# Optimization experiments

Hardware: AMD Instinct MI355X
Metric: run time of the kernel (lower is better)

The kernel has to match this reference:

```python
import jax, jax.numpy as jnp
import numpy as np

B, S, D = 4, 4096, 2048
G, EPG = 4, 16          # num_groups, experts_per_group
E = G * EPG             # num_experts = 64
H = 64                  # complexity estimator hidden


def setup_inputs() -> dict:
    key = jax.random.key(0)
    ks = jax.random.split(key, 7)
    scale = 0.02
    return {
        "x": jax.random.normal(ks[0], (B, S, D), dtype=jnp.float32),
        "Wg": jax.random.normal(ks[1], (G, D), dtype=jnp.float32) * scale,
        "We": jax.random.normal(ks[2], (G, EPG, D), dtype=jnp.float32) * scale,
        "W1": jax.random.normal(ks[3], (H, D), dtype=jnp.float32) * scale,
        "b1": jax.random.normal(ks[4], (H,), dtype=jnp.float32) * scale,
        "W2": jax.random.normal(ks[5], (1, H), dtype=jnp.float32) * scale,
        "b2": jax.random.normal(ks[6], (1,), dtype=jnp.float32) * scale,
        "min_experts": 1,
        "max_experts": 2,
    }


def _router_forward(x, Wg, We, W1, b1, W2, b2, min_experts, max_experts):
    # complexity estimator: Linear -> ReLU -> Linear -> Sigmoid, squeeze(-1)
    h = jax.nn.relu(jnp.einsum("bsd,hd->bsh", x, W1) + b1)
    complexity = jax.nn.sigmoid(jnp.einsum("bsh,oh->bso", h, W2) + b2)[..., 0]  # [B,S]
    # torch: clamp((score * max_experts).int(), min, max); .int() truncates (floor for >=0)
    k = jnp.clip((complexity * max_experts).astype(jnp.int32), min_experts, max_experts)  # [B,S]

    # group routing
    group_logits = jnp.einsum("bsd,gd->bsg", x, Wg)          # [B,S,G]
    group_probs = jax.nn.softmax(group_logits, axis=-1)
    gidx = jnp.argmax(group_probs, axis=-1)                   # [B,S]

    # per-group expert logits for all groups, then pick the chosen group per token
    expert_logits_all = jnp.einsum("bsd,ged->bsge", x, We)    # [B,S,G,EPG]
    expert_logits = jnp.take_along_axis(
        expert_logits_all, gidx[:, :, None, None], axis=2
    )[:, :, 0, :]                                             # [B,S,EPG]
    expert_probs = jax.nn.softmax(expert_logits, axis=-1)     # [B,S,EPG]

    # per-token top-k (k in {1,2}); always take top-2, mask the 2nd when k==1
    topv, topi = jax.lax.top_k(expert_probs, max_experts)     # [B,S,2]
    use2 = (k >= 2).astype(topv.dtype)                        # [B,S]
    mask = jnp.stack([jnp.ones_like(use2), use2], axis=-1)    # [B,S,2]
    denom = jnp.sum(topv * mask, axis=-1, keepdims=True)
    norm_probs = topv * mask / denom                          # [B,S,2]

    flat_idx = gidx[:, :, None] * EPG + topi                  # [B,S,2] global expert ids
    oh = jax.nn.one_hot(flat_idx, E, dtype=x.dtype)           # [B,S,2,E]
    dispatch = jnp.sum(oh * mask[..., None], axis=2)          # [B,S,E]
    combine = jnp.sum(oh * norm_probs[..., None], axis=2)     # [B,S,E]

    # router_probs: group_prob[gidx] * expert_probs scattered into chosen group's slice
    gp_max = jnp.take_along_axis(group_probs, gidx[..., None], axis=-1)[..., 0]  # [B,S]
    oh_g = jax.nn.one_hot(gidx, G, dtype=x.dtype)             # [B,S,G]
    router_probs = (oh_g[..., :, None] * (gp_max[..., None] * expert_probs)[..., None, :]
                    ).reshape(x.shape[0], x.shape[1], E)      # [B,S,E]

    denom_tok = x.shape[0] * x.shape[1]
    router_prob_per_expert = jnp.sum(router_probs, axis=(0, 1)) / denom_tok
    expert_usage = jnp.sum(dispatch, axis=(0, 1)) / denom_tok
    aux_loss = jnp.sum(router_prob_per_expert * expert_usage) * E
    return dispatch, combine, router_probs, aux_loss


def reference(x, Wg, We, W1, b1, W2, b2, min_experts, max_experts):
    return _router_forward(x, Wg, We, W1, b1, W2, b2, min_experts, max_experts)
```

## Files before the change

### kernel.cpp

```cpp
#include <hip/hip_runtime.h>
#include <cmath>

#define T_TOKENS 16384
#define DIM 2048
#define NG 4
#define EPG 16
#define NE 64
#define NJ2 68
#define NT2 5
#define NJP2 80
#define BM 256
#define KS 4
#define KSL (DIM / KS)
#define NITER (KSL / 32)
#define TAU 0.02f

#define XBUF_B 32768
#define WBUF_B 5120

typedef __attribute__((ext_vector_type(8))) short bf16x8;
typedef __attribute__((ext_vector_type(4))) float f32x4;

#define WF_FLOATS (64 * NT2 * 64 * 4)
#define P_OFF WF_FLOATS
#define P_FLOATS ((size_t)KS * T_TOKENS * NJP2)
#define SUM_OFF (P_OFF + P_FLOATS)
#define CNT_OFF (SUM_OFF + 128)
#define LIST_OFF (CNT_OFF + 4)

static __device__ inline unsigned bf16rne(float x) {
    unsigned u = __float_as_uint(x);
    return (u + 0x7FFFu + ((u >> 16) & 1u)) >> 16;
}

#define GLOAD_LDS(gsrc, ldst) \
    __builtin_amdgcn_global_load_lds( \
        (const __attribute__((address_space(1))) void*)(gsrc), \
        (__attribute__((address_space(3))) void*)(ldst), 16, 0, 0)

__global__ void moe_prep(const float* __restrict__ Wg, const float* __restrict__ We,
                         float* __restrict__ ws, float* __restrict__ sums,
                         int* __restrict__ cnt) {
    int bid = blockIdx.x;
    int kstep = bid / NT2, nt = bid % NT2;
    int lane = threadIdx.x;
    if (bid == 0) {
        sums[lane] = 0.f; sums[64 + lane] = 0.f;
        if (lane == 0) *cnt = 0;
    }
    int row = nt * 16 + (lane & 15);
    int k0 = kstep * 32 + (lane >> 4) * 8;
    const float* src = nullptr;
    if (row < NG)        src = Wg + (size_t)row * DIM;
    else if (row < NJ2)  src = We + (size_t)(row - NG) * DIM;
    unsigned r0 = 0, r1 = 0, r2 = 0, r3 = 0;
    if (src) {
        r0 = bf16rne(src[k0 + 0]) | (bf16rne(src[k0 + 1]) << 16);
        r1 = bf16rne(src[k0 + 2]) | (bf16rne(src[k0 + 3]) << 16);
        r2 = bf16rne(src[k0 + 4]) | (bf16rne(src[k0 + 5]) << 16);
        r3 = bf16rne(src[k0 + 6]) | (bf16rne(src[k0 + 7]) << 16);
    }
    ((uint4*)ws)[(size_t)(kstep * NT2 + nt) * 64 + lane] = make_uint4(r0, r1, r2, r3);
}

__global__ __launch_bounds__(512, 1) void moe_gemm(
    const float* __restrict__ x, const float* __restrict__ wfrag,
    float* __restrict__ part) {
    __shared__ __align__(16) char xs[2][XBUF_B];
    __shared__ __align__(16) char wsb[2][WBUF_B];

    const int bid = blockIdx.x;
    const int tg = bid & 63, ks = bid >> 6;
    const int tid = threadIdx.x;
    const int wave = tid >> 6, lane = tid & 63;
    const int l15 = lane & 15, lq = lane >> 4;
    const int T0 = tg * BM;
    const int K0 = ks * KSL;

    const int xtokb = wave * 32 + (lane >> 3);
    const int xp = lane & 7;
    const uint4* wg = (const uint4*)wfrag;

    const int mt0 = wave * 2;
    const int t0 = mt0 * 16 + l15;
    const int t1 = t0 + 16;

    f32x4 acc[2][NT2];
    #pragma unroll
    for (int m = 0; m < 2; ++m)
        #pragma unroll
        for (int n = 0; n < NT2; ++n) acc[m][n] = (f32x4){0.f, 0.f, 0.f, 0.f};

    auto stage = [&](int it) {
        char* xb = xs[it & 1];
        char* wb = wsb[it & 1];
        const int kf = K0 + it * 32;
        #pragma unroll
        for (int j = 0; j < 4; ++j) {
            const int tok = xtokb + j * 8;
            const float* src = x + (size_t)(T0 + tok) * DIM + kf + ((xp ^ (tok & 7)) << 2);
            GLOAD_LDS(src, xb + (wave * 256 + j * 64) * 16);
        }
        if (wave < NT2) {
            const int kstep = ks * NITER + it;
            GLOAD_LDS(wg + ((size_t)kstep * NT2 + wave) * 64 + lane, wb + wave * 1024);
        }
    };

    stage(0);
    #pragma unroll 1
    for (int it = 0; it < NITER; ++it) {
        __syncthreads();
        if (it + 1 < NITER) stage(it + 1);
        const char* xb = xs[it & 1];
        const char* wb = wsb[it & 1];

        union { unsigned u[4]; bf16x8 v; } a0, a1;
        {
            uint4 lo = *(const uint4*)(xb + t0 * 128 + (((lq * 2) ^ (t0 & 7)) << 4));
            uint4 hi = *(const uint4*)(xb + t0 * 128 + (((lq * 2 + 1) ^ (t0 & 7)) << 4));
            a0.u[0] = (lo.x >> 16) | (lo.y & 0xFFFF0000u);
            a0.u[1] = (lo.z >> 16) | (lo.w & 0xFFFF0000u);
            a0.u[2] = (hi.x >> 16) | (hi.y & 0xFFFF0000u);
            a0.u[3] = (hi.z >> 16) | (hi.w & 0xFFFF0000u);
        }
        {
            uint4 lo = *(const uint4*)(xb + t1 * 128 + (((lq * 2) ^ (t1 & 7)) << 4));
            uint4 hi = *(const uint4*)(xb + t1 * 128 + (((lq * 2 + 1) ^ (t1 & 7)) << 4));
            a1.u[0] = (lo.x >> 16) | (lo.y & 0xFFFF0000u);
            a1.u[1] = (lo.z >> 16) | (lo.w & 0xFFFF0000u);
            a1.u[2] = (hi.x >> 16) | (hi.y & 0xFFFF0000u);
            a1.u[3] = (hi.z >> 16) | (hi.w & 0xFFFF0000u);
        }
        #pragma unroll
        for (int n = 0; n < NT2; ++n) {
            bf16x8 bv = *(const bf16x8*)(wb + n * 1024 + lane * 16);
            acc[0][n] = __builtin_amdgcn_mfma_f32_16x16x32_bf16(a0.v, bv, acc[0][n], 0, 0, 0);
            acc[1][n] = __builtin_amdgcn_mfma_f32_16x16x32_bf16(a1.v, bv, acc[1][n], 0, 0, 0);
        }
    }

    float* po = part + (size_t)ks * T_TOKENS * NJP2;
    #pragma unroll
    for (int m = 0; m < 2; ++m) {
        const int tokb = T0 + (mt0 + m) * 16 + lq * 4;
        #pragma unroll
        for (int n = 0; n < NT2; ++n)
            #pragma unroll
            for (int r = 0; r < 4; ++r)
                po[(size_t)(tokb + r) * NJP2 + n * 16 + l15] = acc[m][n][r];
    }
}

__global__ __launch_bounds__(256, 2) void moe_epi(
    const float* __restrict__ part, float* __restrict__ out,
    float* __restrict__ sums, int* __restrict__ cnt, int4* __restrict__ list) {
    __shared__ float slog[16][81];
    __shared__ float rp_s[16 * 17];
    __shared__ int   sc_e1[16];
    __shared__ float s_usage[NE], s_rp[NE];

    const int tid = threadIdx.x;
    const int T0 = blockIdx.x * 16;
    if (tid < NE) { s_usage[tid] = 0.f; s_rp[tid] = 0.f; }

    for (int idx = tid; idx < 16 * NJP2; idx += 256) {
        int t = idx / NJP2, j = idx % NJP2;
        float v = part[(size_t)(T0 + t) * NJP2 + j];
        #pragma unroll
        for (int p = 1; p < KS; ++p)
            v += part[(size_t)p * T_TOKENS * NJP2 + (size_t)(T0 + t) * NJP2 + j];
        slog[t][j] = v;
    }
    __syncthreads();

    {
        const int t = tid >> 4;
        const int q = tid & 15;
        const int tok = T0 + t;
        const float* o = slog[t];

        float gl0 = o[0], gl1 = o[1], gl2 = o[2], gl3 = o[3];
        float gm = gl0; int gi = 0;
        if (gl1 > gm) { gm = gl1; gi = 1; }
        if (gl2 > gm) { gm = gl2; gi = 2; }
        if (gl3 > gm) { gm = gl3; gi = 3; }
        float g2 = -INFINITY;
        if (gi != 0 && gl0 > g2) g2 = gl0;
        if (gi != 1 && gl1 > g2) g2 = gl1;
        if (gi != 2 && gl2 > g2) g2 = gl2;
        if (gi != 3 && gl3 > g2) g2 = gl3;
        bool flagG = (gm - g2) < TAU;
        float gsum = expf(gl0 - gm) + expf(gl1 - gm) + expf(gl2 - gm) + expf(gl3 - gm);
        float gp = 1.f / gsum;

        float el = o[NG + gi * EPG + q];
        float v1v = el; int i1 = q;
        #pragma unroll
        for (int off = 8; off; off >>= 1) {
            float ov = __shfl_xor(v1v, off, 16);
            int   oi = __shfl_xor(i1, off, 16);
            if (ov > v1v || (ov == v1v && oi < i1)) { v1v = ov; i1 = oi; }
        }
        float v2v = (q == i1) ? -INFINITY : el;
        #pragma unroll
        for (int off = 8; off; off >>= 1)
            v2v = fmaxf(v2v, __shfl_xor(v2v, off, 16));
        bool flagE = (v1v - v2v) < TAU;

        float ep = expf(el - v1v);
        float es = ep;
        #pragma unroll
        for (int off = 8; off; off >>= 1) es += __shfl_xor(es, off, 16);
        float inv = 1.f / es;
        rp_s[t * 17 + q] = gp * ep * inv;

        if (q == 0) {
            sc_e1[t] = gi * EPG + i1;
            if (flagG || flagE) {
                int p = atomicAdd(cnt, 1);
                list[p] = make_int4(tok, 0, 0, 0);
            }
        }
    }
    __syncthreads();

    float* outD = out;
    float* outC = out + (size_t)T_TOKENS * NE;
    float* outR = out + (size_t)2 * T_TOKENS * NE;
    for (int idx = tid; idx < 16 * NE; idx += 256) {
        int t = idx >> 6, e = idx & 63;
        int e1i = sc_e1[t];
        int gi = e1i >> 4;
        float disp = (e == e1i) ? 1.f : 0.f;
        float rpv  = ((e >> 4) == gi) ? rp_s[t * 17 + (e & 15)] : 0.f;
        size_t ob = (size_t)(T0 + t) * NE + e;
        outD[ob] = disp; outC[ob] = disp; outR[ob] = rpv;
        atomicAdd(&s_usage[e], disp);
        atomicAdd(&s_rp[e], rpv);
    }
    __syncthreads();
    if (tid < NE) {
        atomicAdd(&sums[tid], s_usage[tid]);
        atomicAdd(&sums[NE + tid], s_rp[tid]);
    }
}

__global__ __launch_bounds__(256, 4) void moe_fix(
    const float* __restrict__ x, const float* __restrict__ Wg,
    const float* __restrict__ We, float* __restrict__ out,
    float* __restrict__ sums, const int* __restrict__ cnt,
    const int4* __restrict__ list) {
    __shared__ float gl_s[NG];
    __shared__ float el_s[EPG];
    __shared__ float rp_row[EPG];
    __shared__ int   s_gi, s_e1;
    __shared__ float s_gp;

    const int tid = threadIdx.x;
    const int wave = tid >> 6, lane = tid & 63;
    const int n = *cnt;

    for (int i = blockIdx.x; i < n; i += gridDim.x) {
        const int tok = list[i].x;
        const float* xrow = x + (size_t)tok * DIM;
        float xr[32];
        #pragma unroll
        for (int m = 0; m < 32; ++m) xr[m] = xrow[lane + m * 64];

        auto dotf = [&](const float* w) -> float {
            float s = 0.f;
            #pragma unroll
            for (int m = 0; m < 32; ++m) s = fmaf(xr[m], w[lane + m * 64], s);
            #pragma unroll
            for (int off = 32; off; off >>= 1) s += __shfl_xor(s, off, 64);
            return s;
        };

        {
            float g = dotf(Wg + (size_t)wave * DIM);
            if (lane == 0) gl_s[wave] = g;
        }
        __syncthreads();

        if (tid == 0) {
            float gm = -INFINITY; int gi = 0;
            #pragma unroll
            for (int g = 0; g < NG; ++g)
                if (gl_s[g] > gm) { gm = gl_s[g]; gi = g; }
            float gsum = 0.f;
            #pragma unroll
            for (int g = 0; g < NG; ++g) gsum += expf(gl_s[g] - gm);
            s_gp = 1.f / gsum;
            s_gi = gi;
        }
        __syncthreads();

        const int gi = s_gi;
        for (int j = wave; j < EPG; j += 4) {
            float e = dotf(We + (size_t)(gi * EPG + j) * DIM);
            if (lane == 0) el_s[j] = e;
        }
        __syncthreads();

        if (tid == 0) {
            float e1 = -INFINITY; int i1 = 0;
            #pragma unroll
            for (int j = 0; j < EPG; ++j)
                if (el_s[j] > e1) { e1 = el_s[j]; i1 = j; }
            float es = 0.f;
            #pragma unroll
            for (int j = 0; j < EPG; ++j) {
                float e = expf(el_s[j] - e1);
                rp_row[j] = e;
                es += e;
            }
            float sc = s_gp / es;
            #pragma unroll
            for (int j = 0; j < EPG; ++j) rp_row[j] *= sc;
            s_e1 = gi * EPG + i1;
        }
        __syncthreads();

        if (tid < NE) {
            const int e = tid;
            float newD = (e == s_e1) ? 1.f : 0.f;
            float newR = ((e >> 4) == gi) ? rp_row[e & 15] : 0.f;
            size_t ob = (size_t)tok * NE + e;
            float oldD = out[ob];
            float oldR = out[(size_t)2 * T_TOKENS * NE + ob];
            out[ob] = newD;
            out[(size_t)T_TOKENS * NE + ob] = newD;
            out[(size_t)2 * T_TOKENS * NE + ob] = newR;
            float dD = newD - oldD, dR = newR - oldR;
            if (dD != 0.f) atomicAdd(&sums[e], dD);
            if (dR != 0.f) atomicAdd(&sums[NE + e], dR);
        }
        __syncthreads();
    }
}

__global__ void moe_finalize(const float* __restrict__ sums, float* __restrict__ out) {
    int l = threadIdx.x;
    float v = sums[l] * sums[NE + l];
    #pragma unroll
    for (int off = 32; off; off >>= 1) v += __shfl_down(v, off, 64);
    if (l == 0) {
        float N = (float)T_TOKENS;
        out[(size_t)3 * T_TOKENS * NE] = v * (float)NE / (N * N);
    }
}

extern "C" void kernel_launch(void* const* d_in, const int* in_sizes, int n_in,
                              void* d_out, int out_size, void* d_ws, size_t ws_size,
                              hipStream_t stream) {
    const float* x  = (const float*)d_in[0];
    const float* Wg = (const float*)d_in[1];
    const float* We = (const float*)d_in[2];
    float* out = (float*)d_out;
    float* ws  = (float*)d_ws;

    float* wfrag = ws;
    float* part  = ws + P_OFF;
    float* sums  = ws + SUM_OFF;
    int*   cnt   = (int*)(ws + CNT_OFF);
    int4*  list  = (int4*)(ws + LIST_OFF);

    moe_prep<<<64 * NT2, 64, 0, stream>>>(Wg, We, wfrag, sums, cnt);
    moe_gemm<<<64 * KS, 512, 0, stream>>>(x, wfrag, part);
    moe_epi<<<T_TOKENS / 16, 256, 0, stream>>>(part, out, sums, cnt, list);
    moe_fix<<<1024, 256, 0, stream>>>(x, Wg, We, out, sums, cnt, list);
    moe_finalize<<<1, 64, 0, stream>>>(sums, out);
}
```

Before: 87.93 us.

## Shrink GEMM token tile to 64 and split N tiles across waves

Reduces the token tile per block from 256 to 64, which launches four times as many blocks with smaller LDS buffers and a launch bound that allows 4 blocks per CU. Waves are now split over 4 M-tiles and 2 halves of the N dimension (3+2 tiles), instead of each wave computing 2 M-tiles across all 5 N tiles. Block indexing is reordered so K-split blocks for the same tokens are adjacent. The aim is higher occupancy and better latency hiding for the memory-bound x stream. In exchange, each block reuses the weight fragments across fewer tokens, and the N split leaves waves with uneven MFMA work.

Result: faster. 85.38 us (-2.9%).

```diff
diff --git a/kernel.cpp b/kernel.cpp
--- a/kernel.cpp
+++ b/kernel.cpp
@@ -9,13 +9,13 @@
 #define NJ2 68
 #define NT2 5
 #define NJP2 80
-#define BM 256
+#define BM 64
 #define KS 4
 #define KSL (DIM / KS)
 #define NITER (KSL / 32)
 #define TAU 0.02f
 
-#define XBUF_B 32768
+#define XBUF_B 8192
 #define WBUF_B 5120
 
 typedef __attribute__((ext_vector_type(8))) short bf16x8;
@@ -63,44 +63,38 @@
     ((uint4*)ws)[(size_t)(kstep * NT2 + nt) * 64 + lane] = make_uint4(r0, r1, r2, r3);
 }
 
-__global__ __launch_bounds__(512, 1) void moe_gemm(
+__global__ __launch_bounds__(512, 4) void moe_gemm(
     const float* __restrict__ x, const float* __restrict__ wfrag,
     float* __restrict__ part) {
     __shared__ __align__(16) char xs[2][XBUF_B];
     __shared__ __align__(16) char wsb[2][WBUF_B];
 
     const int bid = blockIdx.x;
-    const int tg = bid & 63, ks = bid >> 6;
+    const int tg = bid >> 2, ks = bid & 3;
     const int tid = threadIdx.x;
     const int wave = tid >> 6, lane = tid & 63;
     const int l15 = lane & 15, lq = lane >> 4;
     const int T0 = tg * BM;
     const int K0 = ks * KSL;
 
-    const int xtokb = wave * 32 + (lane >> 3);
-    const int xp = lane & 7;
+    const int xtok = wave * 8 + (lane >> 3);
+    const float* xsrc = x + (size_t)(T0 + xtok) * DIM + K0
+                      + (((lane & 7) ^ (lane >> 3)) << 2);
     const uint4* wg = (const uint4*)wfrag;
 
-    const int mt0 = wave * 2;
-    const int t0 = mt0 * 16 + l15;
-    const int t1 = t0 + 16;
-
-    f32x4 acc[2][NT2];
-    #pragma unroll
-    for (int m = 0; m < 2; ++m)
-        #pragma unroll
-        for (int n = 0; n < NT2; ++n) acc[m][n] = (f32x4){0.f, 0.f, 0.f, 0.f};
+    const int mt = wave & 3, nh = wave >> 2;
+    const int ctok = mt * 16 + l15;
+    const int csw = ctok & 7;
+
+    f32x4 acc[3];
+    acc[0] = (f32x4){0.f,0.f,0.f,0.f};
+    acc[1] = (f32x4){0.f,0.f,0.f,0.f};
+    acc[2] = (f32x4){0.f,0.f,0.f,0.f};
 
     auto stage = [&](int it) {
         char* xb = xs[it & 1];
         char* wb = wsb[it & 1];
-        const int kf = K0 + it * 32;
-        #pragma unroll
-        for (int j = 0; j < 4; ++j) {
-            const int tok = xtokb + j * 8;
-            const float* src = x + (size_t)(T0 + tok) * DIM + kf + ((xp ^ (tok & 7)) << 2);
-            GLOAD_LDS(src, xb + (wave * 256 + j * 64) * 16);
-        }
+        GLOAD_LDS(xsrc + it * 32, xb + wave * 1024);
         if (wave < NT2) {
             const int kstep = ks * NITER + it;
             GLOAD_LDS(wg + ((size_t)kstep * NT2 + wave) * 64 + lane, wb + wave * 1024);
@@ -115,40 +109,41 @@
         const char* xb = xs[it & 1];
         const char* wb = wsb[it & 1];
 
-        union { unsigned u[4]; bf16x8 v; } a0, a1;
+        union { unsigned u[4]; bf16x8 v; } af;
         {
-            uint4 lo = *(const uint4*)(xb + t0 * 128 + (((lq * 2) ^ (t0 & 7)) << 4));
-            uint4 hi = *(const uint4*)(xb + t0 * 128 + (((lq * 2 + 1) ^ (t0 & 7)) << 4));
-            a0.u[0] = (lo.x >> 16) | (lo.y & 0xFFFF0000u);
-            a0.u[1] = (lo.z >> 16) | (lo.w & 0xFFFF0000u);
-            a0.u[2] = (hi.x >> 16) | (hi.y & 0xFFFF0000u);
-            a0.u[3] = (hi.z >> 16) | (hi.w & 0xFFFF0000u);
-        }
-        {
-            uint4 lo = *(const uint4*)(xb + t1 * 128 + (((lq * 2) ^ (t1 & 7)) << 4));
-            uint4 hi = *(const uint4*)(xb + t1 * 128 + (((lq * 2 + 1) ^ (t1 & 7)) << 4));
-            a1.u[0] = (lo.x >> 16) | (lo.y & 0xFFFF0000u);
-            a1.u[1] = (lo.z >> 16) | (lo.w & 0xFFFF0000u);
-            a1.u[2] = (hi.x >> 16) | (hi.y & 0xFFFF0000u);
-            a1.u[3] = (hi.z >> 16) | (hi.w & 0xFFFF0000u);
-        }
-        #pragma unroll
-        for (int n = 0; n < NT2; ++n) {
-            bf16x8 bv = *(const bf16x8*)(wb + n * 1024 + lane * 16);
-            acc[0][n] = __builtin_amdgcn_mfma_f32_16x16x32_bf16(a0.v, bv, acc[0][n], 0, 0, 0);
-            acc[1][n] = __builtin_amdgcn_mfma_f32_16x16x32_bf16(a1.v, bv, acc[1][n], 0, 0, 0);
-        }
-    }
-
-    float* po = part + (size_t)ks * T_TOKENS * NJP2;
+            uint4 lo = *(const uint4*)(xb + ctok * 128 + (((lq * 2) ^ csw) << 4));
+            uint4 hi = *(const uint4*)(xb + ctok * 128 + (((lq * 2 + 1) ^ csw) << 4));
+            af.u[0] = (lo.x >> 16) | (lo.y & 0xFFFF0000u);
+            af.u[1] = (lo.z >> 16) | (lo.w & 0xFFFF0000u);
+            af.u[2] = (hi.x >> 16) | (hi.y & 0xFFFF0000u);
+            af.u[3] = (hi.z >> 16) | (hi.w & 0xFFFF0000u);
+        }
+        if (nh == 0) {
+            bf16x8 b0 = *(const bf16x8*)(wb + 0 * 1024 + lane * 16);
+            bf16x8 b1 = *(const bf16x8*)(wb + 1 * 1024 + lane * 16);
+            bf16x8 b2 = *(const bf16x8*)(wb + 2 * 1024 + lane * 16);
+            acc[0] = __builtin_amdgcn_mfma_f32_16x16x32_bf16(af.v, b0, acc[0], 0, 0, 0);
+            acc[1] = __builtin_amdgcn_mfma_f32_16x16x32_bf16(af.v, b1, acc[1], 0, 0, 0);
+            acc[2] = __builtin_amdgcn_mfma_f32_16x16x32_bf16(af.v, b2, acc[2], 0, 0, 0);
+        } else {
+            bf16x8 b0 = *(const bf16x8*)(wb + 3 * 1024 + lane * 16);
+            bf16x8 b1 = *(const bf16x8*)(wb + 4 * 1024 + lane * 16);
+            acc[0] = __builtin_amdgcn_mfma_f32_16x16x32_bf16(af.v, b0, acc[0], 0, 0, 0);
+            acc[1] = __builtin_amdgcn_mfma_f32_16x16x32_bf16(af.v, b1, acc[1], 0, 0, 0);
+        }
+    }
+
+    float* po = part + (size_t)ks * T_TOKENS * NJP2
+              + (size_t)(T0 + mt * 16 + lq * 4) * NJP2 + l15;
+    const int ntb = (nh == 0) ? 0 : 3;
+    const int ntn = (nh == 0) ? 3 : 2;
     #pragma unroll
-    for (int m = 0; m < 2; ++m) {
-        const int tokb = T0 + (mt0 + m) * 16 + lq * 4;
-        #pragma unroll
-        for (int n = 0; n < NT2; ++n)
+    for (int n = 0; n < 3; ++n) {
+        if (n < ntn) {
             #pragma unroll
             for (int r = 0; r < 4; ++r)
-                po[(size_t)(tokb + r) * NJP2 + n * 16 + l15] = acc[m][n][r];
+                po[(size_t)r * NJP2 + (ntb + n) * 16] = acc[n][r];
+        }
     }
 }
 
@@ -367,7 +362,7 @@
     int4*  list  = (int4*)(ws + LIST_OFF);
 
     moe_prep<<<64 * NT2, 64, 0, stream>>>(Wg, We, wfrag, sums, cnt);
-    moe_gemm<<<64 * KS, 512, 0, stream>>>(x, wfrag, part);
+    moe_gemm<<<(T_TOKENS / BM) * KS, 512, 0, stream>>>(x, wfrag, part);
     moe_epi<<<T_TOKENS / 16, 256, 0, stream>>>(part, out, sums, cnt, list);
     moe_fix<<<1024, 256, 0, stream>>>(x, Wg, We, out, sums, cnt, list);
     moe_finalize<<<1, 64, 0, stream>>>(sums, out);
```
